# Kernel tuning notes

Measured on AMD Instinct MI355X. Metric: run time of the kernel, lower is better.

Reference implementation:

```python
import jax, jax.numpy as jnp
import numpy as np

B, S, D, H = 16, 2048, 1024, 1024
WINDOW = 2


def setup_inputs() -> dict:
    key = jax.random.key(0)
    k1, k2 = jax.random.split(key)
    X = jax.random.normal(k1, (B, S, D), dtype=jnp.float32)
    hidden = jnp.zeros((B, H), dtype=jnp.float32)  # initial hidden state (None -> zeros, same math)
    # Linear(window*input_size, 3*hidden_size) weights (torch layout: [out, in])
    W = jax.random.normal(k2, (3 * H, WINDOW * D), dtype=jnp.float32) * (1.0 / np.sqrt(WINDOW * D))
    b = jnp.zeros((3 * H,), dtype=jnp.float32)
    return {"X": X, "hidden": hidden, "W": W, "b": b}


def reference(X, hidden, W, b):
    # X: (B, S, D) -> (S, B, D) as in torch permute(1, 0, 2)
    Xs = jnp.transpose(X, (1, 0, 2))
    # window == 2: concat current token with previous token (zero-padded at t=0)
    Xm1 = jnp.concatenate([jnp.zeros_like(Xs[:1]), Xs[:-1]], axis=0)
    source = jnp.concatenate([Xs, Xm1], axis=2)  # (S, B, 2D)
    Y = jnp.einsum('sbd,hd->sbh', source, W) + b  # (S, B, 3H)
    Z, F, O = jnp.split(Y, 3, axis=2)
    Z = jnp.tanh(Z)
    F = jax.nn.sigmoid(F)

    # ForgetMult: c_t = f_t * z_t + (1 - f_t) * c_{t-1}  (diagonal linear recurrence)
    def step(c, fz):
        f, z = fz
        c = f * z + (1.0 - f) * c
        return c, c

    c_last, C = jax.lax.scan(step, hidden, (F, Z))  # C: (S, B, H)
    Hout = jax.nn.sigmoid(O) * C  # output gate (QRNN-fo)
    return Hout, c_last
```

## Files before the change

kernel.cpp:

```cpp
#include <hip/hip_runtime.h>
#include <hip/hip_bf16.h>
#include <cstdint>
#include <cstddef>


typedef _Float16 f16;
typedef _Float16 f16x2 __attribute__((ext_vector_type(2)));
typedef _Float16 f16x4 __attribute__((ext_vector_type(4)));
typedef _Float16 f16x8 __attribute__((ext_vector_type(8)));
typedef float f32x4 __attribute__((ext_vector_type(4)));

#define Bb 16
#define Ss 2048
#define Dd 1024
#define Hh 1024
#define Nn (3 * Hh)
#define Kk (2 * Dd)
#define BH (Bb * Hh)
#define NCH 16
#define CL 128
#define NQ 8192

__device__ __forceinline__ void gl_lds16(const void* g, void* l) {
  __builtin_amdgcn_global_load_lds(
      (const __attribute__((address_space(1))) void*)g,
      (__attribute__((address_space(3))) void*)l, 16, 0, 0);
}

__global__ void cvt_f32_f16(const float* __restrict__ in, f16* __restrict__ out, int n4) {
  int i = blockIdx.x * blockDim.x + threadIdx.x;
  if (i < n4) {
    const float4 v = ((const float4*)in)[i];
    f16x4 h;
    h[0] = (f16)v.x; h[1] = (f16)v.y; h[2] = (f16)v.z; h[3] = (f16)v.w;
    ((f16x4*)out)[i] = h;
  }
}

__global__ __launch_bounds__(256, 4)
void gemm_gates(const f16* __restrict__ Xh,
                const f16* __restrict__ Wh,
                const float* __restrict__ bias,
                const f16* __restrict__ zblk,
                f16* __restrict__ Zg, f16* __restrict__ Fg, f16* __restrict__ Og) {
  __shared__ __align__(16) f16 As[128 * 64];
  __shared__ __align__(16) f16 Bs[128 * 64];

  const int tid  = threadIdx.x;
  const int wave = tid >> 6;
  const int lane = tid & 63;
  const int bn = blockIdx.x;
  const int bm = blockIdx.y;
  const int m0 = bm * 128;
  const int n0 = bn * 128;

  const int wm = (wave >> 1) * 64;
  const int wn = (wave & 1) * 64;
  const int r  = lane & 15;
  const int q  = lane >> 4;

  const int srl  = lane >> 3;
  const int sseg = ((lane & 7) ^ srl) * 8;

  int as_[4], ab_[4];
#pragma unroll
  for (int i = 0; i < 4; ++i) {
    int mrow = m0 + wave * 32 + i * 8 + srl;
    as_[i] = mrow >> 4;
    ab_[i] = mrow & 15;
  }

  f32x4 acc[4][4];
#pragma unroll
  for (int i = 0; i < 4; ++i)
#pragma unroll
    for (int j = 0; j < 4; ++j)
      acc[i][j] = {0.f, 0.f, 0.f, 0.f};

  for (int kt = 0; kt < 32; ++kt) {
    const int kf = kt * 64;
    __syncthreads();
#pragma unroll
    for (int i = 0; i < 4; ++i) {
      const int row0 = wave * 32 + i * 8;
      const f16* gp;
      if (kf < 1024) {
        gp = Xh + (size_t)ab_[i] * (Ss * Dd) + as_[i] * Dd + kf + sseg;
      } else if (as_[i] > 0) {
        gp = Xh + (size_t)ab_[i] * (Ss * Dd) + (as_[i] - 1) * Dd + (kf - 1024) + sseg;
      } else {
        gp = zblk + sseg;
      }
      gl_lds16(gp, &As[row0 * 64]);
    }
#pragma unroll
    for (int i = 0; i < 4; ++i) {
      const int row0 = wave * 32 + i * 8;
      const f16* gp = Wh + (size_t)(n0 + row0 + srl) * Kk + kf + sseg;
      gl_lds16(gp, &Bs[row0 * 64]);
    }
    __syncthreads();
#pragma unroll
    for (int kk = 0; kk < 64; kk += 32) {
      f16x8 af[4], bf[4];
#pragma unroll
      for (int mi = 0; mi < 4; ++mi) {
        const int row = wm + mi * 16 + r;
        const int seg = ((kk >> 3) + q) ^ (row & 7);
        af[mi] = *(const f16x8*)&As[row * 64 + seg * 8];
      }
#pragma unroll
      for (int ni = 0; ni < 4; ++ni) {
        const int row = wn + ni * 16 + r;
        const int seg = ((kk >> 3) + q) ^ (row & 7);
        bf[ni] = *(const f16x8*)&Bs[row * 64 + seg * 8];
      }
#pragma unroll
      for (int mi = 0; mi < 4; ++mi)
#pragma unroll
        for (int ni = 0; ni < 4; ++ni)
          acc[mi][ni] =
              __builtin_amdgcn_mfma_f32_16x16x32_f16(af[mi], bf[ni], acc[mi][ni], 0, 0, 0);
    }
  }

  const int gate = n0 >> 10;
  f16* gp_out = (gate == 0) ? Zg : ((gate == 1) ? Fg : Og);
#pragma unroll
  for (int ni = 0; ni < 4; ++ni) {
    const int gcol = n0 + wn + ni * 16 + r;
    const int h = gcol & 1023;
    const float bv = bias[gcol];
#pragma unroll
    for (int mi = 0; mi < 4; ++mi) {
#pragma unroll
      for (int reg = 0; reg < 4; ++reg) {
        const int grow = m0 + wm + mi * 16 + q * 4 + reg;
        const int s = grow >> 4, bb = grow & 15;
        const float y = acc[mi][ni][reg] + bv;
        float v;
        if (gate == 0) v = 2.f / (1.f + __expf(-2.f * y)) - 1.f;
        else           v = 1.f / (1.f + __expf(-y));
        gp_out[(size_t)s * BH + bb * Hh + h] = (f16)v;
      }
    }
  }
}

__global__ __launch_bounds__(256, 4)
void chunk_reduce(const f16* __restrict__ Zg, const f16* __restrict__ Fg,
                  float* __restrict__ Apart, float* __restrict__ Bpart) {
  const int idx = blockIdx.x * 256 + threadIdx.x;
  const int q = idx & (NQ - 1);
  const int p = idx >> 13;
  const int base = p * CL;
  constexpr int U = 16;
  f16x2 zb[2][U], fb[2][U];
#pragma unroll
  for (int i = 0; i < U; ++i) {
    zb[0][i] = ((const f16x2*)(Zg + (size_t)(base + i) * BH))[q];
    fb[0][i] = ((const f16x2*)(Fg + (size_t)(base + i) * BH))[q];
  }
  float a0 = 1.f, a1 = 1.f, c0 = 0.f, c1 = 0.f;
  for (int t = 0; t < CL; t += 2 * U) {
#pragma unroll
    for (int i = 0; i < U; ++i) {
      zb[1][i] = ((const f16x2*)(Zg + (size_t)(base + t + U + i) * BH))[q];
      fb[1][i] = ((const f16x2*)(Fg + (size_t)(base + t + U + i) * BH))[q];
    }
#pragma unroll
    for (int i = 0; i < U; ++i) {
      const float f0 = (float)fb[0][i][0], f1 = (float)fb[0][i][1];
      const float z0 = (float)zb[0][i][0], z1 = (float)zb[0][i][1];
      c0 = fmaf(f0, z0 - c0, c0); c1 = fmaf(f1, z1 - c1, c1);
      a0 *= 1.f - f0; a1 *= 1.f - f1;
    }
    if (t + 2 * U < CL) {
#pragma unroll
      for (int i = 0; i < U; ++i) {
        zb[0][i] = ((const f16x2*)(Zg + (size_t)(base + t + 2 * U + i) * BH))[q];
        fb[0][i] = ((const f16x2*)(Fg + (size_t)(base + t + 2 * U + i) * BH))[q];
      }
    }
#pragma unroll
    for (int i = 0; i < U; ++i) {
      const float f0 = (float)fb[1][i][0], f1 = (float)fb[1][i][1];
      const float z0 = (float)zb[1][i][0], z1 = (float)zb[1][i][1];
      c0 = fmaf(f0, z0 - c0, c0); c1 = fmaf(f1, z1 - c1, c1);
      a0 *= 1.f - f0; a1 *= 1.f - f1;
    }
  }
  ((float2*)Apart)[(size_t)p * NQ + q] = make_float2(a0, a1);
  ((float2*)Bpart)[(size_t)p * NQ + q] = make_float2(c0, c1);
}

__global__ __launch_bounds__(256)
void chunk_scan(const float* __restrict__ Apart, const float* __restrict__ Bpart,
                const float* __restrict__ hidden, float* __restrict__ Cin,
                float* __restrict__ out) {
  const int q = blockIdx.x * 256 + threadIdx.x;
  float2 c = ((const float2*)hidden)[q];
#pragma unroll
  for (int p = 0; p < NCH; ++p) {
    ((float2*)Cin)[(size_t)p * NQ + q] = c;
    const float2 a = ((const float2*)Apart)[(size_t)p * NQ + q];
    const float2 b = ((const float2*)Bpart)[(size_t)p * NQ + q];
    c.x = fmaf(a.x, c.x, b.x);
    c.y = fmaf(a.y, c.y, b.y);
  }
  ((float2*)(out + (size_t)Ss * BH))[q] = c;
}

__global__ __launch_bounds__(256, 4)
void chunk_apply(const f16* __restrict__ Zg, const f16* __restrict__ Fg,
                 const f16* __restrict__ Og, const float* __restrict__ Cin,
                 float* __restrict__ out) {
  const int idx = blockIdx.x * 256 + threadIdx.x;
  const int q = idx & (NQ - 1);
  const int p = idx >> 13;
  const int base = p * CL;
  constexpr int U = 16;
  f16x2 zb[2][U], fb[2][U], ob[2][U];
#pragma unroll
  for (int i = 0; i < U; ++i) {
    zb[0][i] = ((const f16x2*)(Zg + (size_t)(base + i) * BH))[q];
    fb[0][i] = ((const f16x2*)(Fg + (size_t)(base + i) * BH))[q];
    ob[0][i] = ((const f16x2*)(Og + (size_t)(base + i) * BH))[q];
  }
  float2 c = ((const float2*)Cin)[(size_t)p * NQ + q];
  for (int t = 0; t < CL; t += 2 * U) {
#pragma unroll
    for (int i = 0; i < U; ++i) {
      zb[1][i] = ((const f16x2*)(Zg + (size_t)(base + t + U + i) * BH))[q];
      fb[1][i] = ((const f16x2*)(Fg + (size_t)(base + t + U + i) * BH))[q];
      ob[1][i] = ((const f16x2*)(Og + (size_t)(base + t + U + i) * BH))[q];
    }
#pragma unroll
    for (int i = 0; i < U; ++i) {
      const float f0 = (float)fb[0][i][0], f1 = (float)fb[0][i][1];
      const float z0 = (float)zb[0][i][0], z1 = (float)zb[0][i][1];
      c.x = fmaf(f0, z0 - c.x, c.x); c.y = fmaf(f1, z1 - c.y, c.y);
      ((float2*)(out + (size_t)(base + t + i) * BH))[q] =
          make_float2((float)ob[0][i][0] * c.x, (float)ob[0][i][1] * c.y);
    }
    if (t + 2 * U < CL) {
#pragma unroll
      for (int i = 0; i < U; ++i) {
        zb[0][i] = ((const f16x2*)(Zg + (size_t)(base + t + 2 * U + i) * BH))[q];
        fb[0][i] = ((const f16x2*)(Fg + (size_t)(base + t + 2 * U + i) * BH))[q];
        ob[0][i] = ((const f16x2*)(Og + (size_t)(base + t + 2 * U + i) * BH))[q];
      }
    }
#pragma unroll
    for (int i = 0; i < U; ++i) {
      const float f0 = (float)fb[1][i][0], f1 = (float)fb[1][i][1];
      const float z0 = (float)zb[1][i][0], z1 = (float)zb[1][i][1];
      c.x = fmaf(f0, z0 - c.x, c.x); c.y = fmaf(f1, z1 - c.y, c.y);
      ((float2*)(out + (size_t)(base + t + U + i) * BH))[q] =
          make_float2((float)ob[1][i][0] * c.x, (float)ob[1][i][1] * c.y);
    }
  }
}

extern "C" void kernel_launch(void* const* d_in, const int* in_sizes, int n_in,
                              void* d_out, int out_size, void* d_ws, size_t ws_size,
                              hipStream_t stream) {
  const float* X      = (const float*)d_in[0];
  const float* hidden = (const float*)d_in[1];
  const float* W      = (const float*)d_in[2];
  const float* bias   = (const float*)d_in[3];
  float* out = (float*)d_out;

  char* ws = (char*)d_ws;
  f16* zblk = (f16*)ws;
  f16* Wh = (f16*)(ws + 256);
  f16* Xh = (f16*)(ws + 256 + 12582912);
  f16* Zg = (f16*)(ws + 256 + 12582912 + 67108864);
  f16* Fg = (f16*)(ws + 256 + 12582912 + 2 * 67108864);
  f16* Og = (f16*)(ws + 256 + 12582912 + 3 * 67108864);
  float* Apart = (float*)(ws + 256 + 12582912 + 4 * 67108864);
  float* Bpart = Apart + NCH * BH;
  float* Cin   = Bpart + NCH * BH;

  hipMemsetAsync(zblk, 0, 256, stream);

  {
    int n4 = (Nn * Kk) / 4;
    cvt_f32_f16<<<(n4 + 255) / 256, 256, 0, stream>>>(W, Wh, n4);
  }
  {
    int n4 = (Bb * Ss * Dd) / 4;
    cvt_f32_f16<<<(n4 + 255) / 256, 256, 0, stream>>>(X, Xh, n4);
  }
  gemm_gates<<<dim3(24, 256), 256, 0, stream>>>(Xh, Wh, bias, zblk, Zg, Fg, Og);
  chunk_reduce<<<(NCH * NQ) / 256, 256, 0, stream>>>(Zg, Fg, Apart, Bpart);
  chunk_scan<<<NQ / 256, 256, 0, stream>>>(Apart, Bpart, hidden, Cin, out);
  chunk_apply<<<(NCH * NQ) / 256, 256, 0, stream>>>(Zg, Fg, Og, Cin, out);
}
```

Before: 729.0 us.

## Rewrite gate GEMM as 256x256 double-buffered pipelined tile with swizzled block order

Rewrites the gate GEMM to use 256x256 output tiles with 512 threads and double-buffered LDS. Global-to-LDS loads for the next k-step are interleaved with MFMA phases, using explicit barriers, waitcnts and setprio. Blocks are remapped with an XCD-aware swizzle, and the zero padding for t=0 is handled by offsetting into a zero region placed before Xh. The aim is to hide load latency and raise MFMA utilisation, at the cost of more LDS and registers per block and fragile hand-tuned synchronization.

```diff
diff --git a/kernel.cpp b/kernel.cpp
--- a/kernel.cpp
+++ b/kernel.cpp
@@ -20,6 +20,11 @@
 #define NCH 16
 #define CL 128
 #define NQ 8192
+#define NT 32
+
+#define BAR() do { asm volatile("" ::: "memory"); __builtin_amdgcn_s_barrier(); asm volatile("" ::: "memory"); } while (0)
+#define LGKM0() asm volatile("s_waitcnt lgkmcnt(0)" ::: "memory")
+#define VMW(n) asm volatile("s_waitcnt vmcnt(" #n ")" ::: "memory")
 
 __device__ __forceinline__ void gl_lds16(const void* g, void* l) {
   __builtin_amdgcn_global_load_lds(
@@ -37,111 +42,200 @@
   }
 }
 
-__global__ __launch_bounds__(256, 4)
+__device__ __forceinline__ void read4(const f16* __restrict__ P, int rbase, int kkv,
+                                      int r, int q, f16x8 fr[4]) {
+#pragma unroll
+  for (int i = 0; i < 4; ++i) {
+    const int row = rbase + i * 16 + r;
+    const int seg = ((kkv >> 3) + q) ^ (row & 7);
+    fr[i] = *(const f16x8*)(P + row * 64 + seg * 8);
+  }
+}
+
+__device__ __forceinline__ void mfma16(const f16x8 af[4], const f16x8 bf[4],
+                                       f32x4 (*acc)[4]) {
+#pragma unroll
+  for (int mi = 0; mi < 4; ++mi)
+#pragma unroll
+    for (int ni = 0; ni < 4; ++ni)
+      acc[mi][ni] = __builtin_amdgcn_mfma_f32_16x16x32_f16(af[mi], bf[ni], acc[mi][ni], 0, 0, 0);
+}
+
+__global__ __launch_bounds__(512, 2)
 void gemm_gates(const f16* __restrict__ Xh,
                 const f16* __restrict__ Wh,
                 const float* __restrict__ bias,
-                const f16* __restrict__ zblk,
                 f16* __restrict__ Zg, f16* __restrict__ Fg, f16* __restrict__ Og) {
-  __shared__ __align__(16) f16 As[128 * 64];
-  __shared__ __align__(16) f16 Bs[128 * 64];
+  __shared__ __align__(16) f16 As[2][256 * 64];
+  __shared__ __align__(16) f16 Bs[2][256 * 64];
 
   const int tid  = threadIdx.x;
   const int wave = tid >> 6;
   const int lane = tid & 63;
-  const int bn = blockIdx.x;
-  const int bm = blockIdx.y;
-  const int m0 = bm * 128;
-  const int n0 = bn * 128;
-
-  const int wm = (wave >> 1) * 64;
-  const int wn = (wave & 1) * 64;
-  const int r  = lane & 15;
-  const int q  = lane >> 4;
-
-  const int srl  = lane >> 3;
-  const int sseg = ((lane & 7) ^ srl) * 8;
-
-  int as_[4], ab_[4];
-#pragma unroll
-  for (int i = 0; i < 4; ++i) {
-    int mrow = m0 + wave * 32 + i * 8 + srl;
-    as_[i] = mrow >> 4;
-    ab_[i] = mrow & 15;
-  }
-
-  f32x4 acc[4][4];
-#pragma unroll
-  for (int i = 0; i < 4; ++i)
+
+  const int bid = blockIdx.x;
+  const int v = (bid & 7) * 192 + (bid >> 3);
+  const int bm = v / 12, bn = v - bm * 12;
+  const int m0 = bm << 8, n0 = bn << 8;
+
+  const int wmBase = (wave >> 2) * 128;
+  const int wnBase = (wave & 3) * 64;
+  const int r = lane & 15, q = lane >> 4;
+
+  const int srl   = lane >> 3;
+  const int sseg8 = ((lane & 7) ^ srl) * 8;
+
+  int oAeC[2], oAeP[2], oAoC[2], oAoP[2], oB0[2], oB1[2];
+  int dAe[2], dAo[2], dB0[2], dB1[2];
+#pragma unroll
+  for (int j = 0; j < 2; ++j) {
+    const int idx = wave * 2 + j;
+    const int t0e = ((idx & 8) << 4) + ((idx & 7) << 3);
+    dAe[j] = t0e * 64;
+    dAo[j] = dAe[j] + 4096;
+    dB0[j] = idx * 512;
+    dB1[j] = dB0[j] + 8192;
+    const int m = m0 + t0e + srl;
+    const int s = m >> 4, b = m & 15;
+    oAeC[j] = b * (Ss * Dd) + s * Dd + sseg8;
+    oAeP[j] = (s > 0) ? (oAeC[j] - Dd - 1024)
+                      : (sseg8 - 3072);
+    oAoC[j] = oAeC[j] + 4 * Dd;
+    oAoP[j] = oAeC[j] + 3 * Dd - 1024;
+    const int n = n0 + idx * 8 + srl;
+    oB0[j] = n * Kk + sseg8;
+    oB1[j] = oB0[j] + 128 * Kk;
+  }
+
+  f32x4 acc[8][4];
+#pragma unroll
+  for (int i = 0; i < 8; ++i)
 #pragma unroll
     for (int j = 0; j < 4; ++j)
       acc[i][j] = {0.f, 0.f, 0.f, 0.f};
 
-  for (int kt = 0; kt < 32; ++kt) {
-    const int kf = kt * 64;
-    __syncthreads();
-#pragma unroll
-    for (int i = 0; i < 4; ++i) {
-      const int row0 = wave * 32 + i * 8;
-      const f16* gp;
-      if (kf < 1024) {
-        gp = Xh + (size_t)ab_[i] * (Ss * Dd) + as_[i] * Dd + kf + sseg;
-      } else if (as_[i] > 0) {
-        gp = Xh + (size_t)ab_[i] * (Ss * Dd) + (as_[i] - 1) * Dd + (kf - 1024) + sseg;
-      } else {
-        gp = zblk + sseg;
-      }
-      gl_lds16(gp, &As[row0 * 64]);
-    }
-#pragma unroll
-    for (int i = 0; i < 4; ++i) {
-      const int row0 = wave * 32 + i * 8;
-      const f16* gp = Wh + (size_t)(n0 + row0 + srl) * Kk + kf + sseg;
-      gl_lds16(gp, &Bs[row0 * 64]);
-    }
-    __syncthreads();
-#pragma unroll
-    for (int kk = 0; kk < 64; kk += 32) {
-      f16x8 af[4], bf[4];
-#pragma unroll
-      for (int mi = 0; mi < 4; ++mi) {
-        const int row = wm + mi * 16 + r;
-        const int seg = ((kk >> 3) + q) ^ (row & 7);
-        af[mi] = *(const f16x8*)&As[row * 64 + seg * 8];
-      }
-#pragma unroll
-      for (int ni = 0; ni < 4; ++ni) {
-        const int row = wn + ni * 16 + r;
-        const int seg = ((kk >> 3) + q) ^ (row & 7);
-        bf[ni] = *(const f16x8*)&Bs[row * 64 + seg * 8];
-      }
-#pragma unroll
-      for (int mi = 0; mi < 4; ++mi)
-#pragma unroll
-        for (int ni = 0; ni < 4; ++ni)
-          acc[mi][ni] =
-              __builtin_amdgcn_mfma_f32_16x16x32_f16(af[mi], bf[ni], acc[mi][ni], 0, 0, 0);
-    }
+  {
+    f16* An = (f16*)As[0]; f16* Bn = (f16*)Bs[0];
+    gl_lds16(Xh + oAeC[0], An + dAe[0]);
+    gl_lds16(Xh + oAeC[1], An + dAe[1]);
+    gl_lds16(Wh + oB0[0],  Bn + dB0[0]);
+    gl_lds16(Wh + oB0[1],  Bn + dB0[1]);
+    gl_lds16(Wh + oB1[0],  Bn + dB1[0]);
+    gl_lds16(Wh + oB1[1],  Bn + dB1[1]);
+    gl_lds16(Xh + oAoC[0], An + dAo[0]);
+    gl_lds16(Xh + oAoC[1], An + dAo[1]);
+  }
+  VMW(2);
+  BAR();
+
+#pragma unroll 1
+  for (int t = 0; t < NT - 1; ++t) {
+    const f16* Ac = As[t & 1];
+    const f16* Bc = Bs[t & 1];
+    f16* An = (f16*)As[(t & 1) ^ 1];
+    f16* Bn = (f16*)Bs[(t & 1) ^ 1];
+    const int kf2 = (t + 1) << 6;
+    int ae0, ae1, ao0, ao1;
+    if (kf2 < 1024) {
+      ae0 = oAeC[0] + kf2; ae1 = oAeC[1] + kf2;
+      ao0 = oAoC[0] + kf2; ao1 = oAoC[1] + kf2;
+    } else {
+      ae0 = oAeP[0] + kf2; ae1 = oAeP[1] + kf2;
+      ao0 = oAoP[0] + kf2; ao1 = oAoP[1] + kf2;
+    }
+    f16x8 af[4], bf0[4], bf1[4];
+
+    read4(Ac, wmBase, 0, r, q, af);
+    read4(Bc, wnBase, 0, r, q, bf0);
+    gl_lds16(Xh + ae0, An + dAe[0]);
+    gl_lds16(Xh + ae1, An + dAe[1]);
+    BAR(); LGKM0();
+    __builtin_amdgcn_s_setprio(1);
+    mfma16(af, bf0, &acc[0]);
+    __builtin_amdgcn_s_setprio(0);
+    BAR();
+
+    read4(Ac, wmBase, 32, r, q, af);
+    read4(Bc, wnBase, 32, r, q, bf1);
+    gl_lds16(Wh + (oB0[0] + kf2), Bn + dB0[0]);
+    gl_lds16(Wh + (oB0[1] + kf2), Bn + dB0[1]);
+    BAR(); LGKM0();
+    __builtin_amdgcn_s_setprio(1);
+    mfma16(af, bf1, &acc[0]);
+    __builtin_amdgcn_s_setprio(0);
+    VMW(4);
+    BAR();
+
+    read4(Ac, wmBase + 64, 0, r, q, af);
+    gl_lds16(Wh + (oB1[0] + kf2), Bn + dB1[0]);
+    gl_lds16(Wh + (oB1[1] + kf2), Bn + dB1[1]);
+    BAR(); LGKM0();
+    __builtin_amdgcn_s_setprio(1);
+    mfma16(af, bf0, &acc[4]);
+    __builtin_amdgcn_s_setprio(0);
+    BAR();
+
+    read4(Ac, wmBase + 64, 32, r, q, af);
+    gl_lds16(Xh + ao0, An + dAo[0]);
+    gl_lds16(Xh + ao1, An + dAo[1]);
+    BAR(); LGKM0();
+    __builtin_amdgcn_s_setprio(1);
+    mfma16(af, bf1, &acc[4]);
+    __builtin_amdgcn_s_setprio(0);
+    VMW(2);
+    BAR();
+  }
+
+  {
+    const f16* Ac = As[1];
+    const f16* Bc = Bs[1];
+    f16x8 af[4], bf0[4], bf1[4];
+    read4(Ac, wmBase, 0, r, q, af);
+    read4(Bc, wnBase, 0, r, q, bf0);
+    BAR(); LGKM0();
+    __builtin_amdgcn_s_setprio(1);
+    mfma16(af, bf0, &acc[0]);
+    __builtin_amdgcn_s_setprio(0);
+    BAR();
+    read4(Ac, wmBase, 32, r, q, af);
+    read4(Bc, wnBase, 32, r, q, bf1);
+    BAR(); LGKM0();
+    __builtin_amdgcn_s_setprio(1);
+    mfma16(af, bf1, &acc[0]);
+    __builtin_amdgcn_s_setprio(0);
+    VMW(0);
+    BAR();
+    read4(Ac, wmBase + 64, 0, r, q, af);
+    BAR(); LGKM0();
+    __builtin_amdgcn_s_setprio(1);
+    mfma16(af, bf0, &acc[4]);
+    __builtin_amdgcn_s_setprio(0);
+    BAR();
+    read4(Ac, wmBase + 64, 32, r, q, af);
+    BAR(); LGKM0();
+    __builtin_amdgcn_s_setprio(1);
+    mfma16(af, bf1, &acc[4]);
+    __builtin_amdgcn_s_setprio(0);
   }
 
   const int gate = n0 >> 10;
   f16* gp_out = (gate == 0) ? Zg : ((gate == 1) ? Fg : Og);
 #pragma unroll
   for (int ni = 0; ni < 4; ++ni) {
-    const int gcol = n0 + wn + ni * 16 + r;
+    const int gcol = n0 + wnBase + ni * 16 + r;
     const int h = gcol & 1023;
     const float bv = bias[gcol];
 #pragma unroll
-    for (int mi = 0; mi < 4; ++mi) {
+    for (int mi = 0; mi < 8; ++mi) {
 #pragma unroll
       for (int reg = 0; reg < 4; ++reg) {
-        const int grow = m0 + wm + mi * 16 + q * 4 + reg;
+        const int grow = m0 + wmBase + mi * 16 + q * 4 + reg;
         const int s = grow >> 4, bb = grow & 15;
         const float y = acc[mi][ni][reg] + bv;
-        float v;
-        if (gate == 0) v = 2.f / (1.f + __expf(-2.f * y)) - 1.f;
-        else           v = 1.f / (1.f + __expf(-y));
-        gp_out[(size_t)s * BH + bb * Hh + h] = (f16)v;
+        float vv;
+        if (gate == 0) vv = 2.f / (1.f + __expf(-2.f * y)) - 1.f;
+        else           vv = 1.f / (1.f + __expf(-y));
+        gp_out[(size_t)s * BH + bb * Hh + h] = (f16)vv;
       }
     }
   }
@@ -272,17 +366,17 @@
   float* out = (float*)d_out;
 
   char* ws = (char*)d_ws;
-  f16* zblk = (f16*)ws;
-  f16* Wh = (f16*)(ws + 256);
-  f16* Xh = (f16*)(ws + 256 + 12582912);
-  f16* Zg = (f16*)(ws + 256 + 12582912 + 67108864);
-  f16* Fg = (f16*)(ws + 256 + 12582912 + 2 * 67108864);
-  f16* Og = (f16*)(ws + 256 + 12582912 + 3 * 67108864);
-  float* Apart = (float*)(ws + 256 + 12582912 + 4 * 67108864);
+  f16* Wh   = (f16*)ws;
+  f16* zpad = (f16*)(ws + 12582912);
+  f16* Xh   = (f16*)(ws + 12582912 + 4096);
+  f16* Zg   = (f16*)(ws + 12582912 + 4096 + 67108864);
+  f16* Fg   = (f16*)(ws + 12582912 + 4096 + 2 * 67108864);
+  f16* Og   = (f16*)(ws + 12582912 + 4096 + 3 * 67108864);
+  float* Apart = (float*)(ws + 12582912 + 4096 + 4 * 67108864);
   float* Bpart = Apart + NCH * BH;
   float* Cin   = Bpart + NCH * BH;
 
-  hipMemsetAsync(zblk, 0, 256, stream);
+  hipMemsetAsync(zpad, 0, 4096, stream);
 
   {
     int n4 = (Nn * Kk) / 4;
@@ -292,7 +386,7 @@
     int n4 = (Bb * Ss * Dd) / 4;
     cvt_f32_f16<<<(n4 + 255) / 256, 256, 0, stream>>>(X, Xh, n4);
   }
-  gemm_gates<<<dim3(24, 256), 256, 0, stream>>>(Xh, Wh, bias, zblk, Zg, Fg, Og);
+  gemm_gates<<<dim3(1536), 512, 0, stream>>>(Xh, Wh, bias, Zg, Fg, Og);
   chunk_reduce<<<(NCH * NQ) / 256, 256, 0, stream>>>(Zg, Fg, Apart, Bpart);
   chunk_scan<<<NQ / 256, 256, 0, stream>>>(Apart, Bpart, hidden, Cin, out);
   chunk_apply<<<(NCH * NQ) / 256, 256, 0, stream>>>(Zg, Fg, Og, Cin, out);
```

New measurement: 775.7 us. 6.4% more time.
